# Optimization experiments

Measured on AMD Instinct MI355X. Metric: run time of the kernel, lower is better.

The kernel has to match this reference:

```python
import jax, jax.numpy as jnp
import numpy as np

SEQ, B, XD = 2048, 4, 16
D, NH, DFF, L, M = 256, 8, 512, 2, 1024
DH = D // NH
NEG_INF = -1e9  # finite stand-in for -inf (same softmax result, grad-safe)


def setup_inputs() -> dict:
    key = jax.random.key(0)
    ks = iter(jax.random.split(key, 40))

    def w(shape, s=0.02):
        return jax.random.normal(next(ks), shape, dtype=jnp.float32) * s

    return {
        "x": jax.random.normal(next(ks), (SEQ, B, XD), dtype=jnp.float32),
        "y": jax.random.normal(next(ks), (SEQ, B), dtype=jnp.float32),
        "single_eval_pos": M,
        "xenc_w": w((D, XD)), "xenc_b": w((D,)),
        "yenc_w": w((D, 1)), "yenc_b": w((D,)),
        "in_proj_w": w((L, 3 * D, D)), "in_proj_b": w((L, 3 * D)),
        "out_proj_w": w((L, D, D)), "out_proj_b": w((L, D)),
        "ln1_g": jnp.ones((L, D), jnp.float32), "ln1_b": jnp.zeros((L, D), jnp.float32),
        "lin1_w": w((L, DFF, D)), "lin1_b": w((L, DFF)),
        "lin2_w": w((L, D, DFF)), "lin2_b": w((L, D)),
        "ln2_g": jnp.ones((L, D), jnp.float32), "ln2_b": jnp.zeros((L, D), jnp.float32),
        "head_w1": w((DFF, D)), "head_b1": w((DFF,)),
        "head_w2": w((1, DFF)), "head_b2": w((1,)),
    }


def _layer_norm(x, g, b, eps=1e-5):
    mu = jnp.mean(x, axis=-1, keepdims=True)
    var = jnp.var(x, axis=-1, keepdims=True)
    return (x - mu) * jax.lax.rsqrt(var + eps) * g + b


def _forward(x, y, M_, p):
    seq, batch = y.shape
    x_src = x @ p["xenc_w"].T + p["xenc_b"]                     # [seq, b, D]
    y_src = y[..., None] @ p["yenc_w"].T + p["yenc_b"]           # [seq, b, D]
    tokens = jnp.concatenate([x_src[:M_] + y_src[:M_], x_src[M_:]], axis=0)

    # prefix-block + diagonal mask: keep (j < M) or (i == j)
    i = jnp.arange(seq)
    keep = (i[None, :] < M_) | (i[:, None] == i[None, :])
    mask = jnp.where(keep, 0.0, NEG_INF).astype(tokens.dtype)    # [seq, seq]

    h = tokens
    for l in range(p["in_proj_w"].shape[0]):
        qkv = h @ p["in_proj_w"][l].T + p["in_proj_b"][l]        # [seq, b, 3D]
        q, k, v = jnp.split(qkv, 3, axis=-1)
        to_heads = lambda t: t.reshape(seq, batch, NH, DH).transpose(1, 2, 0, 3)
        q, k, v = to_heads(q), to_heads(k), to_heads(v)          # [b, h, s, dh]
        scores = jnp.einsum("bhqd,bhkd->bhqk", q, k) / np.float32(np.sqrt(DH)) + mask
        attn = jax.nn.softmax(scores, axis=-1)
        o = jnp.einsum("bhqk,bhkd->bhqd", attn, v)
        o = o.transpose(2, 0, 1, 3).reshape(seq, batch, D)
        o = o @ p["out_proj_w"][l].T + p["out_proj_b"][l]
        h = _layer_norm(h + o, p["ln1_g"][l], p["ln1_b"][l])      # post-norm
        ff = jax.nn.gelu(h @ p["lin1_w"][l].T + p["lin1_b"][l], approximate=False)
        ff = ff @ p["lin2_w"][l].T + p["lin2_b"][l]
        h = _layer_norm(h + ff, p["ln2_g"][l], p["ln2_b"][l])

    q_out = h[M_:]                                               # [seq-M, b, D]
    hid = jax.nn.gelu(q_out @ p["head_w1"].T + p["head_b1"], approximate=False)
    return hid @ p["head_w2"].T + p["head_b2"]                   # [seq-M, b, 1]


def reference(x, y, single_eval_pos, xenc_w, xenc_b, yenc_w, yenc_b,
              in_proj_w, in_proj_b, out_proj_w, out_proj_b,
              ln1_g, ln1_b, lin1_w, lin1_b, lin2_w, lin2_b, ln2_g, ln2_b,
              head_w1, head_b1, head_w2, head_b2):
    p = dict(xenc_w=xenc_w, xenc_b=xenc_b, yenc_w=yenc_w, yenc_b=yenc_b,
             in_proj_w=in_proj_w, in_proj_b=in_proj_b,
             out_proj_w=out_proj_w, out_proj_b=out_proj_b,
             ln1_g=ln1_g, ln1_b=ln1_b, lin1_w=lin1_w, lin1_b=lin1_b,
             lin2_w=lin2_w, lin2_b=lin2_b, ln2_g=ln2_g, ln2_b=ln2_b,
             head_w1=head_w1, head_b1=head_b1, head_w2=head_w2, head_b2=head_b2)
    return _forward(x, y, int(single_eval_pos), p)
```

## Files before the change

kernel.cpp:

```cpp
#include <hip/hip_runtime.h>
#include <hip/hip_bf16.h>
#include <math.h>

#define SEQ    2048
#define BATCH  4
#define XDIM   16
#define DMODEL 256
#define NHEAD  8
#define DH     32
#define DFF    512
#define NLAYER 2
#define MPOS   1024
#define ROWS   (SEQ*BATCH)

#define ATT_SCALE 0.17677669529663687f
#define BK 32

typedef __attribute__((ext_vector_type(8))) short bf16x8;
typedef __attribute__((ext_vector_type(4))) float f32x4;

__device__ __forceinline__ float gelu_exact(float x) {
    return 0.5f * x * (1.0f + erff(x * 0.70710678118654752f));
}
__device__ __forceinline__ short f2bf(float f) {
    unsigned int u = __float_as_uint(f);
    u += 0x7FFFu + ((u >> 16) & 1u);
    return (short)(u >> 16);
}
__device__ __forceinline__ float bf2f(unsigned short u) {
    return __uint_as_float(((unsigned int)u) << 16);
}
__device__ __forceinline__ void gload16(const unsigned short* g, unsigned short* l) {
    __builtin_amdgcn_global_load_lds(
        (const __attribute__((address_space(1))) unsigned int*)g,
        (__attribute__((address_space(3))) unsigned int*)l, 16, 0, 0);
}
#define VMWAIT(N) asm volatile("s_waitcnt vmcnt(" #N ")" ::: "memory")
__device__ __forceinline__ void pipe_barrier() {
    __builtin_amdgcn_sched_barrier(0);
    __builtin_amdgcn_s_barrier();
    __builtin_amdgcn_sched_barrier(0);
}

__global__ __launch_bounds__(256) void encode_cast(
    const float* __restrict__ x, const float* __restrict__ y,
    const float* __restrict__ xw, const float* __restrict__ xb,
    const float* __restrict__ yw, const float* __restrict__ yb,
    float* __restrict__ h, unsigned short* __restrict__ hb,
    const float* __restrict__ s0, const float* __restrict__ s1,
    const float* __restrict__ s2, const float* __restrict__ s3,
    const float* __restrict__ s4,
    unsigned short* __restrict__ d0, unsigned short* __restrict__ d1,
    unsigned short* __restrict__ d2, unsigned short* __restrict__ d3,
    unsigned short* __restrict__ d4)
{
    if (blockIdx.x < ROWS) {
        int row = blockIdx.x;
        int d   = threadIdx.x;
        int s   = row / BATCH;
        __shared__ float xs[XDIM];
        __shared__ float ys;
        if (d < XDIM) xs[d] = x[(size_t)row*XDIM + d];
        if (d == 0)   ys    = y[row];
        __syncthreads();
        float acc = xb[d];
        #pragma unroll
        for (int k = 0; k < XDIM; ++k) acc = fmaf(xs[k], xw[d*XDIM + k], acc);
        if (s < MPOS) acc += ys * yw[d] + yb[d];
        h[(size_t)row*DMODEL + d]  = acc;
        hb[(size_t)row*DMODEL + d] = (unsigned short)f2bf(acc);
        return;
    }
    int i = (blockIdx.x - ROWS)*256 + threadIdx.x;
    if (i >= 147456) return;
    const float* s; unsigned short* d; int off;
    if      (i <  49152) { s = s0; d = d0; off = i; }
    else if (i <  65536) { s = s1; d = d1; off = i - 49152; }
    else if (i <  98304) { s = s2; d = d2; off = i - 65536; }
    else if (i < 131072) { s = s3; d = d3; off = i - 98304; }
    else                 { s = s4; d = d4; off = i - 131072; }
    float4 a = *(const float4*)(s + (size_t)off*8);
    float4 c = *(const float4*)(s + (size_t)off*8 + 4);
    ushort4 u0, u1;
    u0.x=(unsigned short)f2bf(a.x); u0.y=(unsigned short)f2bf(a.y);
    u0.z=(unsigned short)f2bf(a.z); u0.w=(unsigned short)f2bf(a.w);
    u1.x=(unsigned short)f2bf(c.x); u1.y=(unsigned short)f2bf(c.y);
    u1.z=(unsigned short)f2bf(c.z); u1.w=(unsigned short)f2bf(c.w);
    *(ushort4*)(d + (size_t)off*8)     = u0;
    *(ushort4*)(d + (size_t)off*8 + 4) = u1;
}

__global__ __launch_bounds__(256) void gemm_qkv(
    const unsigned short* __restrict__ A, const unsigned short* __restrict__ B,
    const float* __restrict__ bias,
    unsigned short* __restrict__ Qg, unsigned short* __restrict__ Kg,
    unsigned short* __restrict__ Vg, int K)
{
    __shared__ unsigned short As[3][128][BK];
    __shared__ unsigned short Bs[3][64][BK];
    int tid  = threadIdx.x;
    int w    = tid >> 6, lane = tid & 63;
    int col  = lane & 15, quad = lane >> 4;
    int m0   = blockIdx.y * 128, n0 = blockIdx.x * 64;
    int l4   = lane >> 2, c8 = (lane & 3) * 8;

    f32x4 acc[2][4];
    #pragma unroll
    for (int i = 0; i < 2; ++i)
        #pragma unroll
        for (int j = 0; j < 4; ++j) acc[i][j] = (f32x4){0.f,0.f,0.f,0.f};

    const unsigned short* ga = A + (size_t)(m0 + w*32 + l4)*K + c8;
    const unsigned short* gb = B + (size_t)(n0 + w*16 + l4)*K + c8;

    const int NS = K / BK;
    gload16(ga,                  &As[0][w*32     ][0]);
    gload16(ga + (size_t)16*K,   &As[0][w*32 + 16][0]);
    gload16(gb,                  &Bs[0][w*16     ][0]);
    gload16(ga + BK,                  &As[1][w*32     ][0]);
    gload16(ga + BK + (size_t)16*K,   &As[1][w*32 + 16][0]);
    gload16(gb + BK,                  &Bs[1][w*16     ][0]);

    int bcur = 0;
    for (int s = 0; s < NS; ++s) {
        if (s == NS - 1) { VMWAIT(0); } else { VMWAIT(3); }
        pipe_barrier();
        if (s + 2 < NS) {
            int bpre = bcur + 2; if (bpre >= 3) bpre -= 3;
            int k2 = (s + 2) * BK;
            gload16(ga + k2,                &As[bpre][w*32     ][0]);
            gload16(ga + k2 + (size_t)16*K, &As[bpre][w*32 + 16][0]);
            gload16(gb + k2,                &Bs[bpre][w*16     ][0]);
        }
        bf16x8 af[2], bfr[4];
        #pragma unroll
        for (int i = 0; i < 2; ++i) af[i]  = *(const bf16x8*)&As[bcur][w*32 + i*16 + col][quad*8];
        #pragma unroll
        for (int j = 0; j < 4; ++j) bfr[j] = *(const bf16x8*)&Bs[bcur][j*16 + col][quad*8];
        #pragma unroll
        for (int i = 0; i < 2; ++i)
            #pragma unroll
            for (int j = 0; j < 4; ++j)
                acc[i][j] = __builtin_amdgcn_mfma_f32_16x16x32_bf16(bfr[j], af[i], acc[i][j], 0, 0, 0);
        bcur = (bcur == 2) ? 0 : bcur + 1;
    }

    int region = n0 >> 8;
    if (region < 2) {
        #pragma unroll
        for (int i = 0; i < 2; ++i) {
            int m = m0 + w*32 + i*16 + col;
            int s = m >> 2, bidx = m & 3;
            #pragma unroll
            for (int j = 0; j < 4; ++j) {
                int ng = n0 + j*16 + quad*4;
                float4 bi = *(const float4*)&bias[ng];
                ushort4 u;
                u.x=(unsigned short)f2bf(acc[i][j][0] + bi.x);
                u.y=(unsigned short)f2bf(acc[i][j][1] + bi.y);
                u.z=(unsigned short)f2bf(acc[i][j][2] + bi.z);
                u.w=(unsigned short)f2bf(acc[i][j][3] + bi.w);
                int np = ng - (region << 8);
                int hh = np >> 5, d = np & 31;
                int bh = bidx*NHEAD + hh;
                if (region == 0)
                    *(ushort4*)(Qg + ((size_t)(bh*SEQ + s))*DH + d) = u;
                else
                    *(ushort4*)(Kg + ((size_t)(bh*SEQ + s))*DH + d) = u;
            }
        }
    } else {
        __syncthreads();
        unsigned short* T3 = (unsigned short*)As;
        #pragma unroll
        for (int i = 0; i < 2; ++i) {
            int mi = w*32 + i*16 + col;
            int ss = mi >> 2, bidx = mi & 3;
            #pragma unroll
            for (int j = 0; j < 4; ++j) {
                int ni = j*16 + quad*4;
                float4 bi = *(const float4*)&bias[n0 + ni];
                T3[((ni    )*4 + bidx)*32 + ss] = (unsigned short)f2bf(acc[i][j][0] + bi.x);
                T3[((ni + 1)*4 + bidx)*32 + ss] = (unsigned short)f2bf(acc[i][j][1] + bi.y);
                T3[((ni + 2)*4 + bidx)*32 + ss] = (unsigned short)f2bf(acc[i][j][2] + bi.z);
                T3[((ni + 3)*4 + bidx)*32 + ss] = (unsigned short)f2bf(acc[i][j][3] + bi.w);
            }
        }
        __syncthreads();
        int sBase = m0 >> 2;
        #pragma unroll
        for (int r = 0; r < 4; ++r) {
            int chunk = tid + 256*r;
            int l = chunk >> 2, p = chunk & 3;
            int d = l & 31, hh_l = (l >> 5) & 1, bidx = l >> 6;
            int ni = hh_l*32 + d;
            int hh = ((n0 & 255) + ni) >> 5;
            int bh = bidx*NHEAD + hh;
            uint4 val = *(const uint4*)&T3[(ni*4 + bidx)*32 + p*8];
            *(uint4*)(Vg + ((size_t)(bh*DH + d))*SEQ + sBase + p*8) = val;
        }
    }
}

__global__ __launch_bounds__(256) void attn_mfma(
    const unsigned short* __restrict__ Qg,
    const unsigned short* __restrict__ Kg,
    const unsigned short* __restrict__ Vg,
    unsigned short* __restrict__ o)
{
    const int id = blockIdx.x;
    const int sl = id >> 3;
    const int bh = (id & 7) * 4 + (sl >> 5);
    const int qt = sl & 31;
    const int h  = bh & 7;
    const int b  = bh >> 3;
    const int q0 = qt * 64;
    const int tid  = threadIdx.x;
    const int w    = tid >> 6;
    const int lane = tid & 63;
    const int col  = lane & 15;
    const int quad = lane >> 4;

    __shared__ unsigned short Kt[2][64][40];
    __shared__ unsigned short Vt[2][32][72];
    __shared__ unsigned short Pt[4][16][72];

    const int q = q0 + 16*w + col;
    bf16x8 qf = *(const bf16x8*)(Qg + ((size_t)(bh*SEQ + q))*DH + quad*8);

    f32x4 O0 = {0.f,0.f,0.f,0.f};
    f32x4 O1 = {0.f,0.f,0.f,0.f};
    float lsum = 0.f;

    const int kRow = tid >> 2, kCh = (tid & 3) * 8;
    const int vD   = tid >> 3, vCh = (tid & 7) * 8;

    const int nT = 16 + ((q0 >= MPOS) ? 1 : 0);
    uint4 kreg = *(const uint4*)(Kg + ((size_t)(bh*SEQ + kRow))*DH + kCh);
    uint4 vreg = *(const uint4*)(Vg + ((size_t)(bh*DH + vD))*SEQ + vCh);

    for (int kt = 0; kt < nT; ++kt) {
        const bool self = (kt == 16);
        const int  p    = kt & 1;
        *(uint4*)&Kt[p][kRow][kCh] = kreg;
        *(uint4*)&Vt[p][vD][vCh]   = vreg;
        __syncthreads();
        if (kt + 1 < nT) {
            int kn = (kt + 1 == 16) ? q0 : (kt + 1)*64;
            kreg = *(const uint4*)(Kg + ((size_t)(bh*SEQ + kn + kRow))*DH + kCh);
            vreg = *(const uint4*)(Vg + ((size_t)(bh*DH + vD))*SEQ + kn + vCh);
        }

        #pragma unroll
        for (int mt = 0; mt < 4; ++mt) {
            bf16x8 kf = *(const bf16x8*)&Kt[p][mt*16 + col][quad*8];
            f32x4 st = {0.f,0.f,0.f,0.f};
            st = __builtin_amdgcn_mfma_f32_16x16x32_bf16(kf, qf, st, 0, 0, 0);
            ushort4 pw;
            #pragma unroll
            for (int i = 0; i < 4; ++i) {
                float pv = __expf(st[i]*ATT_SCALE);
                if (self && (mt*16 + quad*4 + i != 16*w + col)) pv = 0.f;
                unsigned short us = (unsigned short)f2bf(pv);
                ((unsigned short*)&pw)[i] = us;
                lsum += bf2f(us);
            }
            *(ushort4*)&Pt[w][col][mt*16 + quad*4] = pw;
        }
        #pragma unroll
        for (int c = 0; c < 2; ++c) {
            bf16x8 pf = *(const bf16x8*)&Pt[w][col][c*32 + quad*8];
            bf16x8 v0 = *(const bf16x8*)&Vt[p][col     ][c*32 + quad*8];
            bf16x8 v1 = *(const bf16x8*)&Vt[p][col + 16][c*32 + quad*8];
            O0 = __builtin_amdgcn_mfma_f32_16x16x32_bf16(v0, pf, O0, 0, 0, 0);
            O1 = __builtin_amdgcn_mfma_f32_16x16x32_bf16(v1, pf, O1, 0, 0, 0);
        }
    }

    lsum += __shfl_xor(lsum, 16, 64);
    lsum += __shfl_xor(lsum, 32, 64);
    float inv = 1.0f / lsum;
    ushort4 u0, u1;
    #pragma unroll
    for (int i = 0; i < 4; ++i) {
        ((unsigned short*)&u0)[i] = (unsigned short)f2bf(O0[i]*inv);
        ((unsigned short*)&u1)[i] = (unsigned short)f2bf(O1[i]*inv);
    }
    unsigned short* op = o + ((size_t)(q*BATCH + b))*DMODEL + h*DH;
    *(ushort4*)(op + quad*4)      = u0;
    *(ushort4*)(op + 16 + quad*4) = u1;
}

__global__ __launch_bounds__(256) void mlp_fused(
    const unsigned short* __restrict__ attb,
    const unsigned short* __restrict__ Wout, const float* __restrict__ ob,
    const float* __restrict__ g1, const float* __restrict__ be1,
    const unsigned short* __restrict__ W1, const float* __restrict__ fb1,
    const unsigned short* __restrict__ W2, const float* __restrict__ fb2,
    const float* __restrict__ g2, const float* __restrict__ be2,
    float* __restrict__ h, unsigned short* __restrict__ hb,
    const unsigned short* __restrict__ Wh1, const float* __restrict__ hb1,
    const float* __restrict__ hw2, const float* __restrict__ hb2,
    float* __restrict__ out, int doHead)
{
    __shared__ unsigned short Bs[3][256][BK];
    __shared__ unsigned short As[3][2][16][BK];
    __shared__ unsigned short Ht[2][16][264];
    __shared__ unsigned short Pt[2][16][520];
    __shared__ float sP[2][4][16], qP[2][4][16];

    const int tid  = threadIdx.x;
    const int w    = tid >> 6;
    const int lane = tid & 63;
    const int col  = lane & 15;
    const int quad = lane >> 4;
    const int l4   = lane >> 2;
    const int c8   = (lane & 3) * 8;
    const int bid  = blockIdx.x;
    const int m0a  = bid * 16;
    const int m0b  = 4096 + bid * 16;
    const int ma   = m0a + col;
    const int mb   = m0b + col;

    float resid[2][4][4];

    {
        f32x4 acc[2][4];
        #pragma unroll
        for (int g = 0; g < 2; ++g)
            #pragma unroll
            for (int j = 0; j < 4; ++j) acc[g][j] = (f32x4){0.f,0.f,0.f,0.f};

        const unsigned short* ga0 = attb + (size_t)(m0a + l4)*DMODEL + c8;
        const unsigned short* ga1 = attb + (size_t)(m0b + l4)*DMODEL + c8;
        const unsigned short* gb  = Wout + (size_t)(w*64 + l4)*DMODEL + c8;
        const int NS = DMODEL / BK;

        #pragma unroll
        for (int pb = 0; pb < 2; ++pb) {
            int k = pb * BK;
            if (w == 0) {
                gload16(ga0 + k, &As[pb][0][0][0]);
                gload16(ga1 + k, &As[pb][1][0][0]);
            }
            #pragma unroll
            for (int rr = 0; rr < 4; ++rr)
                gload16(gb + k + (size_t)(rr*16)*DMODEL, &Bs[pb][w*64 + rr*16][0]);
        }
        int bcur = 0;
        for (int s = 0; s < NS; ++s) {
            if (s == NS - 1)  { VMWAIT(0); }
            else if (w == 0)  { VMWAIT(6); }
            else              { VMWAIT(4); }
            pipe_barrier();
            if (s + 2 < NS) {
                int bpre = bcur + 2; if (bpre >= 3) bpre -= 3;
                int k2 = (s + 2) * BK;
                if (w == 0) {
                    gload16(ga0 + k2, &As[bpre][0][0][0]);
                    gload16(ga1 + k2, &As[bpre][1][0][0]);
                }
                #pragma unroll
                for (int rr = 0; rr < 4; ++rr)
                    gload16(gb + k2 + (size_t)(rr*16)*DMODEL, &Bs[bpre][w*64 + rr*16][0]);
            }
            bf16x8 af0 = *(const bf16x8*)&As[bcur][0][col][quad*8];
            bf16x8 af1 = *(const bf16x8*)&As[bcur][1][col][quad*8];
            #pragma unroll
            for (int j = 0; j < 4; ++j) {
                bf16x8 bfr = *(const bf16x8*)&Bs[bcur][w*64 + j*16 + col][quad*8];
                acc[0][j] = __builtin_amdgcn_mfma_f32_16x16x32_bf16(bfr, af0, acc[0][j], 0, 0, 0);
                acc[1][j] = __builtin_amdgcn_mfma_f32_16x16x32_bf16(bfr, af1, acc[1][j], 0, 0, 0);
            }
            bcur = (bcur == 2) ? 0 : bcur + 1;
        }

        float ssum[2] = {0.f, 0.f}, qsum[2] = {0.f, 0.f};
        #pragma unroll
        for (int g = 0; g < 2; ++g) {
            int m = g ? mb : ma;
            #pragma unroll
            for (int j = 0; j < 4; ++j) {
                int n = w*64 + j*16 + quad*4;
                float4 bi = *(const float4*)&ob[n];
                float4 hv = *(const float4*)&h[(size_t)m*DMODEL + n];
                #pragma unroll
                for (int i = 0; i < 4; ++i) {
                    float val = acc[g][j][i] + ((const float*)&bi)[i] + ((const float*)&hv)[i];
                    resid[g][j][i] = val;
                    ssum[g] += val; qsum[g] += val*val;
                }
            }
        }
        #pragma unroll
        for (int g = 0; g < 2; ++g) {
            ssum[g] += __shfl_xor(ssum[g], 16, 64); ssum[g] += __shfl_xor(ssum[g], 32, 64);
            qsum[g] += __shfl_xor(qsum[g], 16, 64); qsum[g] += __shfl_xor(qsum[g], 32, 64);
        }
        if (quad == 0) {
            sP[0][w][col] = ssum[0]; qP[0][w][col] = qsum[0];
            sP[1][w][col] = ssum[1]; qP[1][w][col] = qsum[1];
        }
        __syncthreads();
        #pragma unroll
        for (int g = 0; g < 2; ++g) {
            float st = sP[g][0][col] + sP[g][1][col] + sP[g][2][col] + sP[g][3][col];
            float qt = qP[g][0][col] + qP[g][1][col] + qP[g][2][col] + qP[g][3][col];
            float mu   = st * (1.0f/DMODEL);
            float var  = qt * (1.0f/DMODEL) - mu*mu;
            float rstd = rsqrtf(var + 1e-5f);
            #pragma unroll
            for (int j = 0; j < 4; ++j) {
                int n = w*64 + j*16 + quad*4;
                float4 gv = *(const float4*)&g1[n];
                float4 bv = *(const float4*)&be1[n];
                ushort4 u;
                #pragma unroll
                for (int i = 0; i < 4; ++i) {
                    float o = (resid[g][j][i]-mu)*rstd*((const float*)&gv)[i] + ((const float*)&bv)[i];
                    resid[g][j][i] = o;
                    ((unsigned short*)&u)[i] = (unsigned short)f2bf(o);
                }
                *(ushort4*)&Ht[g][col][n] = u;
            }
        }
        __syncthreads();
    }

    #pragma unroll 1
    for (int nh = 0; nh < 2; ++nh) {
        f32x4 acc[2][4];
        #pragma unroll
        for (int g = 0; g < 2; ++g)
            #pragma unroll
            for (int j = 0; j < 4; ++j) acc[g][j] = (f32x4){0.f,0.f,0.f,0.f};
        const unsigned short* gb = W1 + (size_t)(nh*256 + w*64 + l4)*DMODEL + c8;
        const int NS = DMODEL / BK;

        #pragma unroll
        for (int pb = 0; pb < 2; ++pb)
            #pragma unroll
            for (int rr = 0; rr < 4; ++rr)
                gload16(gb + pb*BK + (size_t)(rr*16)*DMODEL, &Bs[pb][w*64 + rr*16][0]);

        int bcur = 0;
        for (int s = 0; s < NS; ++s) {
            if (s == NS - 1) { VMWAIT(0); } else { VMWAIT(4); }
            pipe_barrier();
            if (s + 2 < NS) {
                int bpre = bcur + 2; if (bpre >= 3) bpre -= 3;
                int k2 = (s + 2) * BK;
                #pragma unroll
                for (int rr = 0; rr < 4; ++rr)
                    gload16(gb + k2 + (size_t)(rr*16)*DMODEL, &Bs[bpre][w*64 + rr*16][0]);
            }
            bf16x8 af0 = *(const bf16x8*)&Ht[0][col][s*BK + quad*8];
            bf16x8 af1 = *(const bf16x8*)&Ht[1][col][s*BK + quad*8];
            #pragma unroll
            for (int j = 0; j < 4; ++j) {
                bf16x8 bfr = *(const bf16x8*)&Bs[bcur][w*64 + j*16 + col][quad*8];
                acc[0][j] = __builtin_amdgcn_mfma_f32_16x16x32_bf16(bfr, af0, acc[0][j], 0, 0, 0);
                acc[1][j] = __builtin_amdgcn_mfma_f32_16x16x32_bf16(bfr, af1, acc[1][j], 0, 0, 0);
            }
            bcur = (bcur == 2) ? 0 : bcur + 1;
        }
        #pragma unroll
        for (int g = 0; g < 2; ++g)
            #pragma unroll
            for (int j = 0; j < 4; ++j) {
                int n2 = nh*256 + w*64 + j*16 + quad*4;
                float4 bi = *(const float4*)&fb1[n2];
                ushort4 u;
                #pragma unroll
                for (int i = 0; i < 4; ++i)
                    ((unsigned short*)&u)[i] = (unsigned short)f2bf(gelu_exact(acc[g][j][i] + ((const float*)&bi)[i]));
                *(ushort4*)&Pt[g][col][n2] = u;
            }
        pipe_barrier();
    }

    {
        __syncthreads();
        f32x4 acc[2][4];
        #pragma unroll
        for (int g = 0; g < 2; ++g)
            #pragma unroll
            for (int j = 0; j < 4; ++j) acc[g][j] = (f32x4){0.f,0.f,0.f,0.f};
        const unsigned short* gb = W2 + (size_t)(w*64 + l4)*DFF + c8;
        const int NS = DFF / BK;

        #pragma unroll
        for (int pb = 0; pb < 2; ++pb)
            #pragma unroll
            for (int rr = 0; rr < 4; ++rr)
                gload16(gb + pb*BK + (size_t)(rr*16)*DFF, &Bs[pb][w*64 + rr*16][0]);

        int bcur = 0;
        for (int s = 0; s < NS; ++s) {
            if (s == NS - 1) { VMWAIT(0); } else { VMWAIT(4); }
            pipe_barrier();
            if (s + 2 < NS) {
                int bpre = bcur + 2; if (bpre >= 3) bpre -= 3;
                int k2 = (s + 2) * BK;
                #pragma unroll
                for (int rr = 0; rr < 4; ++rr)
                    gload16(gb + k2 + (size_t)(rr*16)*DFF, &Bs[bpre][w*64 + rr*16][0]);
            }
            bf16x8 af0 = *(const bf16x8*)&Pt[0][col][s*BK + quad*8];
            bf16x8 af1 = *(const bf16x8*)&Pt[1][col][s*BK + quad*8];
            #pragma unroll
            for (int j = 0; j < 4; ++j) {
                bf16x8 bfr = *(const bf16x8*)&Bs[bcur][w*64 + j*16 + col][quad*8];
                acc[0][j] = __builtin_amdgcn_mfma_f32_16x16x32_bf16(bfr, af0, acc[0][j], 0, 0, 0);
                acc[1][j] = __builtin_amdgcn_mfma_f32_16x16x32_bf16(bfr, af1, acc[1][j], 0, 0, 0);
            }
            bcur = (bcur == 2) ? 0 : bcur + 1;
        }

        float ssum[2] = {0.f, 0.f}, qsum[2] = {0.f, 0.f};
        #pragma unroll
        for (int g = 0; g < 2; ++g)
            #pragma unroll
            for (int j = 0; j < 4; ++j) {
                int n = w*64 + j*16 + quad*4;
                float4 bi = *(const float4*)&fb2[n];
                #pragma unroll
                for (int i = 0; i < 4; ++i) {
                    float val = acc[g][j][i] + ((const float*)&bi)[i] + resid[g][j][i];
                    resid[g][j][i] = val;
                    ssum[g] += val; qsum[g] += val*val;
                }
            }
        #pragma unroll
        for (int g = 0; g < 2; ++g) {
            ssum[g] += __shfl_xor(ssum[g], 16, 64); ssum[g] += __shfl_xor(ssum[g], 32, 64);
            qsum[g] += __shfl_xor(qsum[g], 16, 64); qsum[g] += __shfl_xor(qsum[g], 32, 64);
        }
        if (quad == 0) {
            sP[0][w][col] = ssum[0]; qP[0][w][col] = qsum[0];
            sP[1][w][col] = ssum[1]; qP[1][w][col] = qsum[1];
        }
        __syncthreads();
        #pragma unroll
        for (int g = 0; g < 2; ++g) {
            int m = g ? mb : ma;
            float st = sP[g][0][col] + sP[g][1][col] + sP[g][2][col] + sP[g][3][col];
            float qt = qP[g][0][col] + qP[g][1][col] + qP[g][2][col] + qP[g][3][col];
            float mu   = st * (1.0f/DMODEL);
            float var  = qt * (1.0f/DMODEL) - mu*mu;
            float rstd = rsqrtf(var + 1e-5f);
            #pragma unroll
            for (int j = 0; j < 4; ++j) {
                int n = w*64 + j*16 + quad*4;
                float4 gv = *(const float4*)&g2[n];
                float4 bv = *(const float4*)&be2[n];
                float4 o;
                ushort4 u;
                #pragma unroll
                for (int i = 0; i < 4; ++i) {
                    float ov = (resid[g][j][i]-mu)*rstd*((const float*)&gv)[i] + ((const float*)&bv)[i];
                    ((float*)&o)[i] = ov;
                    ((unsigned short*)&u)[i] = (unsigned short)f2bf(ov);
                }
                *(float4*)&h[(size_t)m*DMODEL + n] = o;
                *(ushort4*)(hb + (size_t)m*DMODEL + n) = u;
                *(ushort4*)&Ht[g][col][n] = u;
            }
        }
        __syncthreads();
    }

    if (doHead) {
        float sdot = 0.f;
        #pragma unroll 1
        for (int nh = 0; nh < 2; ++nh) {
            f32x4 acc[4];
            #pragma unroll
            for (int j = 0; j < 4; ++j) acc[j] = (f32x4){0.f,0.f,0.f,0.f};
            const unsigned short* gb = Wh1 + (size_t)(nh*256 + w*64 + l4)*DMODEL + c8;
            const int NS = DMODEL / BK;

            #pragma unroll
            for (int pb = 0; pb < 2; ++pb)
                #pragma unroll
                for (int rr = 0; rr < 4; ++rr)
                    gload16(gb + pb*BK + (size_t)(rr*16)*DMODEL, &Bs[pb][w*64 + rr*16][0]);

            int bcur = 0;
            for (int s = 0; s < NS; ++s) {
                if (s == NS - 1) { VMWAIT(0); } else { VMWAIT(4); }
                pipe_barrier();
                if (s + 2 < NS) {
                    int bpre = bcur + 2; if (bpre >= 3) bpre -= 3;
                    int k2 = (s + 2) * BK;
                    #pragma unroll
                    for (int rr = 0; rr < 4; ++rr)
                        gload16(gb + k2 + (size_t)(rr*16)*DMODEL, &Bs[bpre][w*64 + rr*16][0]);
                }
                bf16x8 af = *(const bf16x8*)&Ht[1][col][s*BK + quad*8];
                #pragma unroll
                for (int j = 0; j < 4; ++j) {
                    bf16x8 bfr = *(const bf16x8*)&Bs[bcur][w*64 + j*16 + col][quad*8];
                    acc[j] = __builtin_amdgcn_mfma_f32_16x16x32_bf16(bfr, af, acc[j], 0, 0, 0);
                }
                bcur = (bcur == 2) ? 0 : bcur + 1;
            }
            #pragma unroll
            for (int j = 0; j < 4; ++j) {
                int n2 = nh*256 + w*64 + j*16 + quad*4;
                float4 b1v = *(const float4*)&hb1[n2];
                float4 w2v = *(const float4*)&hw2[n2];
                #pragma unroll
                for (int i = 0; i < 4; ++i)
                    sdot += gelu_exact(acc[j][i] + ((const float*)&b1v)[i]) * ((const float*)&w2v)[i];
            }
            pipe_barrier();
        }
        sdot += __shfl_xor(sdot, 16, 64); sdot += __shfl_xor(sdot, 32, 64);
        if (quad == 0) sP[0][w][col] = sdot;
        __syncthreads();
        if (tid < 16)
            out[bid*16 + tid] = sP[0][0][tid] + sP[0][1][tid] + sP[0][2][tid] + sP[0][3][tid] + hb2[0];
    }
}

extern "C" void kernel_launch(void* const* d_in, const int* in_sizes, int n_in,
                              void* d_out, int out_size, void* d_ws, size_t ws_size,
                              hipStream_t stream)
{
    const float* x        = (const float*)d_in[0];
    const float* y        = (const float*)d_in[1];
    const float* xenc_w   = (const float*)d_in[3];
    const float* xenc_b   = (const float*)d_in[4];
    const float* yenc_w   = (const float*)d_in[5];
    const float* yenc_b   = (const float*)d_in[6];
    const float* in_proj_w  = (const float*)d_in[7];
    const float* in_proj_b  = (const float*)d_in[8];
    const float* out_proj_w = (const float*)d_in[9];
    const float* out_proj_b = (const float*)d_in[10];
    const float* ln1_g    = (const float*)d_in[11];
    const float* ln1_b    = (const float*)d_in[12];
    const float* lin1_w   = (const float*)d_in[13];
    const float* lin1_b   = (const float*)d_in[14];
    const float* lin2_w   = (const float*)d_in[15];
    const float* lin2_b   = (const float*)d_in[16];
    const float* ln2_g    = (const float*)d_in[17];
    const float* ln2_b    = (const float*)d_in[18];
    const float* head_w1  = (const float*)d_in[19];
    const float* head_b1  = (const float*)d_in[20];
    const float* head_w2  = (const float*)d_in[21];
    const float* head_b2  = (const float*)d_in[22];
    float* out = (float*)d_out;

    float* ws  = (float*)d_ws;
    float* h    = ws;
    unsigned short* hb    = (unsigned short*)(h + (size_t)ROWS*DMODEL);
    unsigned short* attb  = hb    + (size_t)ROWS*DMODEL;
    unsigned short* Qg    = attb  + (size_t)ROWS*DMODEL;
    unsigned short* Kg    = Qg    + (size_t)BATCH*NHEAD*SEQ*DH;
    unsigned short* Vg    = Kg    + (size_t)BATCH*NHEAD*SEQ*DH;
    unsigned short* Wqkv  = Vg    + (size_t)BATCH*NHEAD*SEQ*DH;
    unsigned short* Wout  = Wqkv  + (size_t)NLAYER*3*DMODEL*DMODEL;
    unsigned short* Wl1   = Wout  + (size_t)NLAYER*DMODEL*DMODEL;
    unsigned short* Wl2   = Wl1   + (size_t)NLAYER*DFF*DMODEL;
    unsigned short* Wh1   = Wl2   + (size_t)NLAYER*DMODEL*DFF;

    encode_cast<<<ROWS + 576, 256, 0, stream>>>(
        x, y, xenc_w, xenc_b, yenc_w, yenc_b, h, hb,
        in_proj_w, out_proj_w, lin1_w, lin2_w, head_w1,
        Wqkv, Wout, Wl1, Wl2, Wh1);

    for (int l = 0; l < NLAYER; ++l) {
        gemm_qkv<<<dim3(12, ROWS/128), 256, 0, stream>>>(
            hb, Wqkv + (size_t)l*3*DMODEL*DMODEL, in_proj_b + l*3*DMODEL,
            Qg, Kg, Vg, DMODEL);
        attn_mfma<<<dim3(SEQ/64 * NHEAD * BATCH), 256, 0, stream>>>(Qg, Kg, Vg, attb);
        mlp_fused<<<256, 256, 0, stream>>>(
            attb,
            Wout + (size_t)l*DMODEL*DMODEL, out_proj_b + l*DMODEL,
            ln1_g + l*DMODEL, ln1_b + l*DMODEL,
            Wl1 + (size_t)l*DFF*DMODEL, lin1_b + l*DFF,
            Wl2 + (size_t)l*DMODEL*DFF, lin2_b + l*DMODEL,
            ln2_g + l*DMODEL, ln2_b + l*DMODEL,
            h, hb,
            Wh1, head_b1, head_w2, head_b2,
            out, (l == NLAYER-1) ? 1 : 0);
    }
}
```

Before: 258.4 us.

## Pair train and test query tiles in attention blocks, remap QKV grid per XCD

The attention kernel now gives each block two query tiles, one from the train prefix and one from the test half. They share each staged K/V tile, so the prefix keys and values are loaded into shared memory once per pair instead of once per tile, and every block runs a uniform 17 iterations. The QKV GEMM uses a 1D grid remapped so that blocks landing on the same XCD cover neighbouring row tiles for L2 locality. The encoder now handles four rows per block and keeps its weights in registers. In exchange, attention runs half as many blocks with higher register and LDS use, which may lower occupancy.

```diff
diff --git a/kernel.cpp b/kernel.cpp
--- a/kernel.cpp
+++ b/kernel.cpp
@@ -54,24 +54,32 @@
     unsigned short* __restrict__ d2, unsigned short* __restrict__ d3,
     unsigned short* __restrict__ d4)
 {
-    if (blockIdx.x < ROWS) {
-        int row = blockIdx.x;
-        int d   = threadIdx.x;
-        int s   = row / BATCH;
-        __shared__ float xs[XDIM];
-        __shared__ float ys;
-        if (d < XDIM) xs[d] = x[(size_t)row*XDIM + d];
-        if (d == 0)   ys    = y[row];
-        __syncthreads();
-        float acc = xb[d];
-        #pragma unroll
-        for (int k = 0; k < XDIM; ++k) acc = fmaf(xs[k], xw[d*XDIM + k], acc);
-        if (s < MPOS) acc += ys * yw[d] + yb[d];
-        h[(size_t)row*DMODEL + d]  = acc;
-        hb[(size_t)row*DMODEL + d] = (unsigned short)f2bf(acc);
+    if (blockIdx.x < ROWS/4) {
+        int g = blockIdx.x;
+        int d = threadIdx.x;
+        __shared__ float xs[4][XDIM];
+        __shared__ float ys[4];
+        if (d < 64) xs[d>>4][d&15] = x[(size_t)(g*4 + (d>>4))*XDIM + (d&15)];
+        if (d < 4)  ys[d] = y[g*4 + d];
+        __syncthreads();
+        float wreg[XDIM];
+        #pragma unroll
+        for (int k = 0; k < XDIM; ++k) wreg[k] = xw[d*XDIM + k];
+        const float xbv = xb[d], ywv = yw[d], ybv = yb[d];
+        const bool train = (g < MPOS);
+        #pragma unroll
+        for (int r = 0; r < 4; ++r) {
+            int row = g*4 + r;
+            float acc = xbv;
+            #pragma unroll
+            for (int k = 0; k < XDIM; ++k) acc = fmaf(xs[r][k], wreg[k], acc);
+            if (train) acc += ys[r]*ywv + ybv;
+            h[(size_t)row*DMODEL + d]  = acc;
+            hb[(size_t)row*DMODEL + d] = (unsigned short)f2bf(acc);
+        }
         return;
     }
-    int i = (blockIdx.x - ROWS)*256 + threadIdx.x;
+    int i = (blockIdx.x - ROWS/4)*256 + threadIdx.x;
     if (i >= 147456) return;
     const float* s; unsigned short* d; int off;
     if      (i <  49152) { s = s0; d = d0; off = i; }
@@ -101,7 +109,9 @@
     int tid  = threadIdx.x;
     int w    = tid >> 6, lane = tid & 63;
     int col  = lane & 15, quad = lane >> 4;
-    int m0   = blockIdx.y * 128, n0 = blockIdx.x * 64;
+    int u    = blockIdx.x >> 3, xcd = blockIdx.x & 7;
+    int by   = xcd*8 + u/12, bx = u%12;
+    int m0   = by * 128, n0 = bx * 64;
     int l4   = lane >> 2, c8 = (lane & 3) * 8;
 
     f32x4 acc[2][4];
@@ -155,18 +165,18 @@
             for (int j = 0; j < 4; ++j) {
                 int ng = n0 + j*16 + quad*4;
                 float4 bi = *(const float4*)&bias[ng];
-                ushort4 u;
-                u.x=(unsigned short)f2bf(acc[i][j][0] + bi.x);
-                u.y=(unsigned short)f2bf(acc[i][j][1] + bi.y);
-                u.z=(unsigned short)f2bf(acc[i][j][2] + bi.z);
-                u.w=(unsigned short)f2bf(acc[i][j][3] + bi.w);
+                ushort4 uu;
+                uu.x=(unsigned short)f2bf(acc[i][j][0] + bi.x);
+                uu.y=(unsigned short)f2bf(acc[i][j][1] + bi.y);
+                uu.z=(unsigned short)f2bf(acc[i][j][2] + bi.z);
+                uu.w=(unsigned short)f2bf(acc[i][j][3] + bi.w);
                 int np = ng - (region << 8);
                 int hh = np >> 5, d = np & 31;
                 int bh = bidx*NHEAD + hh;
                 if (region == 0)
-                    *(ushort4*)(Qg + ((size_t)(bh*SEQ + s))*DH + d) = u;
+                    *(ushort4*)(Qg + ((size_t)(bh*SEQ + s))*DH + d) = uu;
                 else
-                    *(ushort4*)(Kg + ((size_t)(bh*SEQ + s))*DH + d) = u;
+                    *(ushort4*)(Kg + ((size_t)(bh*SEQ + s))*DH + d) = uu;
             }
         }
     } else {
@@ -208,13 +218,14 @@
     const unsigned short* __restrict__ Vg,
     unsigned short* __restrict__ o)
 {
-    const int id = blockIdx.x;
-    const int sl = id >> 3;
-    const int bh = (id & 7) * 4 + (sl >> 5);
-    const int qt = sl & 31;
-    const int h  = bh & 7;
-    const int b  = bh >> 3;
-    const int q0 = qt * 64;
+    const int id  = blockIdx.x;
+    const int sl  = id >> 3;
+    const int bh  = (id & 7) * 4 + (sl >> 4);
+    const int qt2 = sl & 15;
+    const int h   = bh & 7;
+    const int b   = bh >> 3;
+    const int q0A = qt2 * 64;
+    const int q0B = MPOS + qt2 * 64;
     const int tid  = threadIdx.x;
     const int w    = tid >> 6;
     const int lane = tid & 63;
@@ -223,30 +234,32 @@
 
     __shared__ unsigned short Kt[2][64][40];
     __shared__ unsigned short Vt[2][32][72];
-    __shared__ unsigned short Pt[4][16][72];
-
-    const int q = q0 + 16*w + col;
-    bf16x8 qf = *(const bf16x8*)(Qg + ((size_t)(bh*SEQ + q))*DH + quad*8);
-
-    f32x4 O0 = {0.f,0.f,0.f,0.f};
-    f32x4 O1 = {0.f,0.f,0.f,0.f};
-    float lsum = 0.f;
+    __shared__ unsigned short PtA[4][16][72];
+    __shared__ unsigned short PtB[4][16][72];
+
+    const int qA = q0A + 16*w + col;
+    const int qB = q0B + 16*w + col;
+    bf16x8 qfA = *(const bf16x8*)(Qg + ((size_t)(bh*SEQ + qA))*DH + quad*8);
+    bf16x8 qfB = *(const bf16x8*)(Qg + ((size_t)(bh*SEQ + qB))*DH + quad*8);
+
+    f32x4 O0A = {0.f,0.f,0.f,0.f}, O1A = {0.f,0.f,0.f,0.f};
+    f32x4 O0B = {0.f,0.f,0.f,0.f}, O1B = {0.f,0.f,0.f,0.f};
+    float lsumA = 0.f, lsumB = 0.f;
 
     const int kRow = tid >> 2, kCh = (tid & 3) * 8;
     const int vD   = tid >> 3, vCh = (tid & 7) * 8;
 
-    const int nT = 16 + ((q0 >= MPOS) ? 1 : 0);
     uint4 kreg = *(const uint4*)(Kg + ((size_t)(bh*SEQ + kRow))*DH + kCh);
     uint4 vreg = *(const uint4*)(Vg + ((size_t)(bh*DH + vD))*SEQ + vCh);
 
-    for (int kt = 0; kt < nT; ++kt) {
+    for (int kt = 0; kt < 17; ++kt) {
         const bool self = (kt == 16);
         const int  p    = kt & 1;
         *(uint4*)&Kt[p][kRow][kCh] = kreg;
         *(uint4*)&Vt[p][vD][vCh]   = vreg;
         __syncthreads();
-        if (kt + 1 < nT) {
-            int kn = (kt + 1 == 16) ? q0 : (kt + 1)*64;
+        if (kt < 16) {
+            int kn = (kt == 15) ? q0B : (kt + 1)*64;
             kreg = *(const uint4*)(Kg + ((size_t)(bh*SEQ + kn + kRow))*DH + kCh);
             vreg = *(const uint4*)(Vg + ((size_t)(bh*DH + vD))*SEQ + kn + vCh);
         }
@@ -254,41 +267,67 @@
         #pragma unroll
         for (int mt = 0; mt < 4; ++mt) {
             bf16x8 kf = *(const bf16x8*)&Kt[p][mt*16 + col][quad*8];
-            f32x4 st = {0.f,0.f,0.f,0.f};
-            st = __builtin_amdgcn_mfma_f32_16x16x32_bf16(kf, qf, st, 0, 0, 0);
-            ushort4 pw;
+            if (!self) {
+                f32x4 stA = {0.f,0.f,0.f,0.f};
+                stA = __builtin_amdgcn_mfma_f32_16x16x32_bf16(kf, qfA, stA, 0, 0, 0);
+                ushort4 pwA;
+                #pragma unroll
+                for (int i = 0; i < 4; ++i) {
+                    float pv = __expf(stA[i]*ATT_SCALE);
+                    unsigned short us = (unsigned short)f2bf(pv);
+                    ((unsigned short*)&pwA)[i] = us;
+                    lsumA += bf2f(us);
+                }
+                *(ushort4*)&PtA[w][col][mt*16 + quad*4] = pwA;
+            }
+            f32x4 stB = {0.f,0.f,0.f,0.f};
+            stB = __builtin_amdgcn_mfma_f32_16x16x32_bf16(kf, qfB, stB, 0, 0, 0);
+            ushort4 pwB;
             #pragma unroll
             for (int i = 0; i < 4; ++i) {
-                float pv = __expf(st[i]*ATT_SCALE);
+                float pv = __expf(stB[i]*ATT_SCALE);
                 if (self && (mt*16 + quad*4 + i != 16*w + col)) pv = 0.f;
                 unsigned short us = (unsigned short)f2bf(pv);
-                ((unsigned short*)&pw)[i] = us;
-                lsum += bf2f(us);
-            }
-            *(ushort4*)&Pt[w][col][mt*16 + quad*4] = pw;
+                ((unsigned short*)&pwB)[i] = us;
+                lsumB += bf2f(us);
+            }
+            *(ushort4*)&PtB[w][col][mt*16 + quad*4] = pwB;
         }
         #pragma unroll
         for (int c = 0; c < 2; ++c) {
-            bf16x8 pf = *(const bf16x8*)&Pt[w][col][c*32 + quad*8];
             bf16x8 v0 = *(const bf16x8*)&Vt[p][col     ][c*32 + quad*8];
             bf16x8 v1 = *(const bf16x8*)&Vt[p][col + 16][c*32 + quad*8];
-            O0 = __builtin_amdgcn_mfma_f32_16x16x32_bf16(v0, pf, O0, 0, 0, 0);
-            O1 = __builtin_amdgcn_mfma_f32_16x16x32_bf16(v1, pf, O1, 0, 0, 0);
-        }
-    }
-
-    lsum += __shfl_xor(lsum, 16, 64);
-    lsum += __shfl_xor(lsum, 32, 64);
-    float inv = 1.0f / lsum;
+            if (!self) {
+                bf16x8 pfA = *(const bf16x8*)&PtA[w][col][c*32 + quad*8];
+                O0A = __builtin_amdgcn_mfma_f32_16x16x32_bf16(v0, pfA, O0A, 0, 0, 0);
+                O1A = __builtin_amdgcn_mfma_f32_16x16x32_bf16(v1, pfA, O1A, 0, 0, 0);
+            }
+            bf16x8 pfB = *(const bf16x8*)&PtB[w][col][c*32 + quad*8];
+            O0B = __builtin_amdgcn_mfma_f32_16x16x32_bf16(v0, pfB, O0B, 0, 0, 0);
+            O1B = __builtin_amdgcn_mfma_f32_16x16x32_bf16(v1, pfB, O1B, 0, 0, 0);
+        }
+    }
+
+    lsumA += __shfl_xor(lsumA, 16, 64); lsumA += __shfl_xor(lsumA, 32, 64);
+    lsumB += __shfl_xor(lsumB, 16, 64); lsumB += __shfl_xor(lsumB, 32, 64);
+    float invA = 1.0f / lsumA, invB = 1.0f / lsumB;
     ushort4 u0, u1;
     #pragma unroll
     for (int i = 0; i < 4; ++i) {
-        ((unsigned short*)&u0)[i] = (unsigned short)f2bf(O0[i]*inv);
-        ((unsigned short*)&u1)[i] = (unsigned short)f2bf(O1[i]*inv);
-    }
-    unsigned short* op = o + ((size_t)(q*BATCH + b))*DMODEL + h*DH;
-    *(ushort4*)(op + quad*4)      = u0;
-    *(ushort4*)(op + 16 + quad*4) = u1;
+        ((unsigned short*)&u0)[i] = (unsigned short)f2bf(O0A[i]*invA);
+        ((unsigned short*)&u1)[i] = (unsigned short)f2bf(O1A[i]*invA);
+    }
+    unsigned short* opA = o + ((size_t)(qA*BATCH + b))*DMODEL + h*DH;
+    *(ushort4*)(opA + quad*4)      = u0;
+    *(ushort4*)(opA + 16 + quad*4) = u1;
+    #pragma unroll
+    for (int i = 0; i < 4; ++i) {
+        ((unsigned short*)&u0)[i] = (unsigned short)f2bf(O0B[i]*invB);
+        ((unsigned short*)&u1)[i] = (unsigned short)f2bf(O1B[i]*invB);
+    }
+    unsigned short* opB = o + ((size_t)(qB*BATCH + b))*DMODEL + h*DH;
+    *(ushort4*)(opB + quad*4)      = u0;
+    *(ushort4*)(opB + 16 + quad*4) = u1;
 }
 
 __global__ __launch_bounds__(256) void mlp_fused(
@@ -665,16 +704,16 @@
     unsigned short* Wl2   = Wl1   + (size_t)NLAYER*DFF*DMODEL;
     unsigned short* Wh1   = Wl2   + (size_t)NLAYER*DMODEL*DFF;
 
-    encode_cast<<<ROWS + 576, 256, 0, stream>>>(
+    encode_cast<<<ROWS/4 + 576, 256, 0, stream>>>(
         x, y, xenc_w, xenc_b, yenc_w, yenc_b, h, hb,
         in_proj_w, out_proj_w, lin1_w, lin2_w, head_w1,
         Wqkv, Wout, Wl1, Wl2, Wh1);
 
     for (int l = 0; l < NLAYER; ++l) {
-        gemm_qkv<<<dim3(12, ROWS/128), 256, 0, stream>>>(
+        gemm_qkv<<<768, 256, 0, stream>>>(
             hb, Wqkv + (size_t)l*3*DMODEL*DMODEL, in_proj_b + l*3*DMODEL,
             Qg, Kg, Vg, DMODEL);
-        attn_mfma<<<dim3(SEQ/64 * NHEAD * BATCH), 256, 0, stream>>>(Qg, Kg, Vg, attb);
+        attn_mfma<<<512, 256, 0, stream>>>(Qg, Kg, Vg, attb);
         mlp_fused<<<256, 256, 0, stream>>>(
             attb,
             Wout + (size_t)l*DMODEL*DMODEL, out_proj_b + l*DMODEL,
```

Measured after the change: 258.9 us. Within noise of the previous version (+0.2%).
